# Performance work log

Measured on AMD Instinct MI355X. Metric: run time of the kernel, lower is better.

The kernel has to match this reference:

```python
import jax, jax.numpy as jnp
import numpy as np

N_NODES = 50000
N_EDGES = 1_600_000
IN_DIM = 6
EMB = 64
EDGE_DIM = 1
L = 4
BN_EPS = 1e-5


def _bn_relu(x, gamma, beta):
    # BatchNorm1d in training mode: biased batch stats over the row dim.
    mu = jnp.mean(x, axis=0)
    var = jnp.var(x, axis=0)
    xhat = (x - mu) * jax.lax.rsqrt(var + BN_EPS)
    return jax.nn.relu(xhat * gamma + beta)


def setup_inputs() -> dict:
    key = jax.random.key(0)
    ks = jax.random.split(key, 32)
    s = 0.1
    inp = {
        "x": jax.random.normal(ks[0], (N_NODES, IN_DIM), jnp.float32),
        "edge_index": jax.random.randint(ks[1], (2, N_EDGES), 0, N_NODES),
        "edge_attr": jax.random.normal(ks[2], (N_EDGES, EDGE_DIM), jnp.float32),
        "lin_in_W": jax.random.normal(ks[3], (IN_DIM, EMB)) * s,
        "lin_in_b": jnp.zeros((EMB,)),
        # per-layer stacked params, leading dim L
        "msg_W1": jax.random.normal(ks[4], (L, 2 * EMB + EDGE_DIM, EMB)) * s,
        "msg_b1": jnp.zeros((L, EMB)),
        "msg_g1": jnp.ones((L, EMB)),
        "msg_be1": jnp.zeros((L, EMB)),
        "msg_W2": jax.random.normal(ks[5], (L, EMB, EMB)) * s,
        "msg_b2": jnp.zeros((L, EMB)),
        "msg_g2": jnp.ones((L, EMB)),
        "msg_be2": jnp.zeros((L, EMB)),
        "upd_W1": jax.random.normal(ks[6], (L, 2 * EMB, EMB)) * s,
        "upd_b1": jnp.zeros((L, EMB)),
        "upd_g1": jnp.ones((L, EMB)),
        "upd_be1": jnp.zeros((L, EMB)),
        "upd_W2": jax.random.normal(ks[7], (L, EMB, EMB)) * s,
        "upd_b2": jnp.zeros((L, EMB)),
        "upd_g2": jnp.ones((L, EMB)),
        "upd_be2": jnp.zeros((L, EMB)),
        "pred_W": jax.random.normal(ks[8], (EMB, 1)) * s,
        "pred_b": jnp.zeros((1,)),
    }
    return inp


def reference(x, edge_index, edge_attr, lin_in_W, lin_in_b,
              msg_W1, msg_b1, msg_g1, msg_be1, msg_W2, msg_b2, msg_g2, msg_be2,
              upd_W1, upd_b1, upd_g1, upd_be1, upd_W2, upd_b2, upd_g2, upd_be2,
              pred_W, pred_b):
    n = x.shape[0]
    src = edge_index[0]  # j (source)
    dst = edge_index[1]  # i (target / aggregation index)

    h = x @ lin_in_W + lin_in_b  # (n, d)
    for l in range(L):
        h_i = h[dst]                              # (e, d) destination feats
        h_j = h[src]                              # (e, d) source feats
        m = jnp.concatenate([h_i, h_j, edge_attr], axis=-1)  # (e, 2d+de)
        m = _bn_relu(m @ msg_W1[l] + msg_b1[l], msg_g1[l], msg_be1[l])
        m = _bn_relu(m @ msg_W2[l] + msg_b2[l], msg_g2[l], msg_be2[l])
        aggr = jax.ops.segment_sum(m, dst, num_segments=n)   # (n, d)
        u = jnp.concatenate([h, aggr], axis=-1)              # (n, 2d)
        u = _bn_relu(u @ upd_W1[l] + upd_b1[l], upd_g1[l], upd_be1[l])
        u = _bn_relu(u @ upd_W2[l] + upd_b2[l], upd_g2[l], upd_be2[l])
        h = h + u  # residual
    out = h @ pred_W + pred_b
    return out.reshape(-1)
```

## Files before the change

### kernel.cpp

```cpp
#include <hip/hip_runtime.h>
#include <hip/hip_bf16.h>


#define BN_EPS 1e-5f
#define NSH 128
#define LYS 72
#define LW1S 168
#define LW2S 68
#define ASW 66

typedef __attribute__((ext_vector_type(8))) short short8;
typedef __attribute__((ext_vector_type(16))) float floatx16;

#define MFMA32 __builtin_amdgcn_mfma_f32_32x32x16_bf16

__device__ __forceinline__ short f2bs(float f) {
  union { float f; unsigned u; } x; x.f = f;
  unsigned r = x.u + 0x7fffu + ((x.u >> 16) & 1u);
  return (short)(r >> 16);
}
__device__ __forceinline__ short f2bs_fast(float f) {
  union { float f; unsigned u; } x; x.f = f;
  return (short)((x.u + 0x8000u) >> 16);
}
__device__ __forceinline__ float bs2f(short s) {
  union { unsigned u; float f; } x;
  x.u = ((unsigned)(unsigned short)s) << 16;
  return x.f;
}


__global__ void lin_in_kernel(const float* __restrict__ x,
                              const float* __restrict__ W,
                              const float* __restrict__ b, float* __restrict__ h,
                              short* __restrict__ hb, int N) {
  int gid = blockIdx.x * blockDim.x + threadIdx.x;
  if (gid >= N * 64) return;
  int n = gid >> 6, o = gid & 63;
  float acc = b[o];
#pragma unroll
  for (int k = 0; k < 6; ++k) acc += x[n * 6 + k] * W[k * 64 + o];
  h[gid] = acc;
  hb[gid] = f2bs(acc);
}

__global__ void deg_kernel(const int* __restrict__ ei, int* __restrict__ deg,
                           int E) {
  int gid = blockIdx.x * blockDim.x + threadIdx.x;
  if (gid < E) atomicAdd(&deg[ei[E + gid]], 1);
}

__global__ void scan_kernel(const int* __restrict__ deg, int* __restrict__ offs,
                            int N) {
  __shared__ int s[1024];
  int t = threadIdx.x;
  int chunk = (N + 1023) >> 10;
  int lo = t * chunk, hi = lo + chunk;
  if (hi > N) hi = N;
  if (lo > N) lo = N;
  int tot = 0;
  for (int i = lo; i < hi; ++i) tot += deg[i];
  s[t] = tot;
  __syncthreads();
  for (int off = 1; off < 1024; off <<= 1) {
    int v = (t >= off) ? s[t - off] : 0;
    __syncthreads();
    s[t] += v;
    __syncthreads();
  }
  int run = s[t] - tot;
  for (int i = lo; i < hi; ++i) {
    offs[i] = run;
    run += deg[i];
  }
}

__global__ void fill_kernel(const int* __restrict__ ei,
                            const int* __restrict__ offs, int* __restrict__ cnt,
                            int* __restrict__ sorted, int E) {
  int gid = blockIdx.x * blockDim.x + threadIdx.x;
  if (gid >= E) return;
  int d = ei[E + gid];
  int pos = offs[d] + atomicAdd(&cnt[d], 1);
  sorted[pos] = gid;
}

__global__ void gather_edges_kernel(const int* __restrict__ ei,
                                    const int* __restrict__ sorted,
                                    const float* __restrict__ ea,
                                    int* __restrict__ dd, int* __restrict__ ds,
                                    short* __restrict__ es, int E, int Epad) {
  int i = blockIdx.x * 256 + threadIdx.x;
  if (i >= Epad) return;
  if (i < E) {
    int e = sorted[i];
    dd[i] = ei[E + e];
    ds[i] = ei[e];
    es[i] = f2bs(ea[e]);
  } else {
    dd[i] = -1;
    ds[i] = 0;
    es[i] = 0;
  }
}

__global__ void pack_w1_kernel(const float* __restrict__ W,
                               short* __restrict__ Wt, int L_) {
  int i = blockIdx.x * 256 + threadIdx.x;
  if (i >= L_ * 64 * 160) return;
  int k = i % 160, n = (i / 160) % 64, l = i / (160 * 64);
  Wt[i] = (k < 129) ? f2bs(W[((size_t)l * 129 + k) * 64 + n]) : (short)0;
}

__global__ void pack_w2_kernel(const float* __restrict__ W,
                               short* __restrict__ Wt, int L_) {
  int i = blockIdx.x * 256 + threadIdx.x;
  if (i >= L_ * 64 * 64) return;
  int k = i % 64, n = (i / 64) % 64, l = i / 4096;
  Wt[i] = f2bs(W[((size_t)l * 64 + k) * 64 + n]);
}

__global__ void bn_finalize_kernel(const float* __restrict__ shards,
                                   const float* __restrict__ gamma,
                                   const float* __restrict__ beta, float cnt,
                                   float* __restrict__ ac) {
  int o = threadIdx.x;
  float s = 0.f, q = 0.f;
  for (int i = 0; i < NSH; ++i) {
    s += shards[i * 128 + o];
    q += shards[i * 128 + 64 + o];
  }
  float mu = s / cnt;
  float var = fmaxf(q / cnt - mu * mu, 0.f);
  float r = rsqrtf(var + BN_EPS);
  float g = gamma[o];
  ac[o] = g * r;
  ac[64 + o] = beta[o] - mu * g * r;
}

__global__ void bn_finalize_pack1(const float* __restrict__ shards,
                                  const float* __restrict__ gamma,
                                  const float* __restrict__ beta, float cnt,
                                  const float* __restrict__ W,
                                  const float* __restrict__ b,
                                  short* __restrict__ Wt,
                                  float* __restrict__ bs) {
  __shared__ float sa[64];
  int t = threadIdx.x;
  if (t < 64) {
    float s = 0.f, q = 0.f;
    for (int i = 0; i < NSH; ++i) {
      s += shards[i * 128 + t];
      q += shards[i * 128 + 64 + t];
    }
    float mu = s / cnt;
    float var = fmaxf(q / cnt - mu * mu, 0.f);
    float r = rsqrtf(var + BN_EPS);
    float a = gamma[t] * r;
    float c = beta[t] - mu * a;
    sa[t] = a;
    if (blockIdx.x == 0) bs[t] = a * b[t] + c;
  }
  __syncthreads();
  int i = blockIdx.x * 256 + t;
  if (i < 64 * 160) {
    int k = i % 160, n = i / 160;
    Wt[i] = (k < 129) ? f2bs(W[k * 64 + n] * sa[n]) : (short)0;
  }
}

__global__ void bn_finalize_pack2(const float* __restrict__ shards,
                                  const float* __restrict__ gamma,
                                  const float* __restrict__ beta, float cnt,
                                  const float* __restrict__ W,
                                  const float* __restrict__ b,
                                  short* __restrict__ Wt,
                                  float* __restrict__ bs) {
  __shared__ float sa[64];
  int t = threadIdx.x;
  if (t < 64) {
    float s = 0.f, q = 0.f;
    for (int i = 0; i < NSH; ++i) {
      s += shards[i * 128 + t];
      q += shards[i * 128 + 64 + t];
    }
    float mu = s / cnt;
    float var = fmaxf(q / cnt - mu * mu, 0.f);
    float r = rsqrtf(var + BN_EPS);
    float a = gamma[t] * r;
    float c = beta[t] - mu * a;
    sa[t] = a;
    if (blockIdx.x == 0) bs[t] = a * b[t] + c;
  }
  __syncthreads();
  int i = blockIdx.x * 256 + t;
  if (i < 64 * 64) {
    int k = i % 64, n = i / 64;
    Wt[i] = f2bs(W[k * 64 + n] * sa[n]);
  }
}


__device__ __forceinline__ void stage_w1(const short* __restrict__ Wt,
                                         short* Lw, int t) {
#pragma unroll
  for (int i = 0; i < 5; ++i) {
    int c = t + i * 256;
    int col = c / 20, ch = c % 20;
    *(short8*)&Lw[col * LW1S + ch * 8] = *(const short8*)&Wt[col * 160 + ch * 8];
  }
}
__device__ __forceinline__ void stage_w2(const short* __restrict__ Wt,
                                         short* Lw, int t) {
#pragma unroll
  for (int i = 0; i < 2; ++i) {
    int c = t + i * 256;
    int col = c >> 3, ch = c & 7;
    *(short8*)&Lw[col * LW2S + ch * 8] = *(const short8*)&Wt[col * 64 + ch * 8];
  }
}

__device__ __forceinline__ void gemm1_32(const short* __restrict__ hbf,
                                         const short* Lw1,
                                         const float* __restrict__ bias, int d,
                                         int sx, short eav, int me, int hl,
                                         floatx16 acc[2]) {
  const short* hd = hbf + (size_t)d * 64 + hl * 8;
  const short* hs = hbf + (size_t)sx * 64 + hl * 8;
  short8 A[8];
#pragma unroll
  for (int kc = 0; kc < 4; ++kc) A[kc] = *(const short8*)(hd + kc * 16);
#pragma unroll
  for (int kc = 0; kc < 4; ++kc) A[4 + kc] = *(const short8*)(hs + kc * 16);
  short8 a8 = {0, 0, 0, 0, 0, 0, 0, 0};
  if (hl == 0) a8[0] = eav;
#pragma unroll
  for (int nt = 0; nt < 2; ++nt) {
    int col = nt * 32 + me;
    float bv = bias[col];
    floatx16 a;
#pragma unroll
    for (int r = 0; r < 16; ++r) a[r] = bv;
    const short* wp = Lw1 + col * LW1S + hl * 8;
#pragma unroll
    for (int kc = 0; kc < 8; ++kc) {
      short8 B = *(const short8*)(wp + kc * 16);
      a = MFMA32(A[kc], B, a, 0, 0, 0);
    }
    short8 B8 = *(const short8*)(wp + 128);
    a = MFMA32(a8, B8, a, 0, 0, 0);
    acc[nt] = a;
  }
}

__device__ __forceinline__ void gemm2_32(const short* Ly, const short* Lw2,
                                         const float* __restrict__ bias, int w,
                                         int me, int hl, floatx16 acc[2]) {
  short8 Z[4];
  const short* zp = &Ly[(w * 32 + me) * LYS + hl * 8];
#pragma unroll
  for (int kc = 0; kc < 4; ++kc) Z[kc] = *(const short8*)(zp + kc * 16);
#pragma unroll
  for (int nt = 0; nt < 2; ++nt) {
    int col = nt * 32 + me;
    float bv = bias[col];
    floatx16 a;
#pragma unroll
    for (int r = 0; r < 16; ++r) a[r] = bv;
    const short* wp = Lw2 + col * LW2S + hl * 8;
#pragma unroll
    for (int kc = 0; kc < 4; ++kc) {
      short8 B = *(const short8*)(wp + kc * 16);
      a = MFMA32(Z[kc], B, a, 0, 0, 0);
    }
    acc[nt] = a;
  }
}

__device__ __forceinline__ void stats32(const floatx16 acc[2], int idx0, int w,
                                        int hl, int lane, int E, bool full,
                                        float* sredw) {
#pragma unroll
  for (int nt = 0; nt < 2; ++nt) {
    float s = 0.f, q = 0.f;
#pragma unroll
    for (int r = 0; r < 16; ++r) {
      float v = acc[nt][r];
      if (!full) {
        int row = (r & 3) + 8 * (r >> 2) + 4 * hl;
        if (idx0 + w * 32 + row >= E) v = 0.f;
      }
      s += v;
      q += v * v;
    }
    s += __shfl_down(s, 32, 64);
    q += __shfl_down(q, 32, 64);
    if (lane < 32) {
      sredw[nt * 32 + lane] = s;
      sredw[64 + nt * 32 + lane] = q;
    }
  }
}

__device__ __forceinline__ void write_ly(short* Ly, const floatx16 acc[2],
                                         int w, int me, int hl, bool mask,
                                         int idx0, int E) {
#pragma unroll
  for (int nt = 0; nt < 2; ++nt) {
    int col = nt * 32 + me;
#pragma unroll
    for (int r = 0; r < 16; ++r) {
      int row = (r & 3) + 8 * (r >> 2) + 4 * hl;
      float v = fmaxf(acc[nt][r], 0.f);
      if (mask && idx0 + w * 32 + row >= E) v = 0.f;
      Ly[(w * 32 + row) * LYS + col] = f2bs_fast(v);
    }
  }
}


__global__ __launch_bounds__(256) void edge_pass_a(
    const short* __restrict__ hbf, const short* __restrict__ Wt1,
    const float* __restrict__ b1, const int* __restrict__ dd,
    const int* __restrict__ dsr, const short* __restrict__ es,
    float* __restrict__ stat, int E) {
  __shared__ __align__(16) short Lw1[64 * LW1S];
  __shared__ float sred[4][128];
  int t = threadIdx.x, idx0 = blockIdx.x * 128;
  stage_w1(Wt1, Lw1, t);
  __syncthreads();
  int w = t >> 6, lane = t & 63, me = lane & 31, hl = lane >> 5;
  int eg = idx0 + w * 32 + me;
  int d = dd[eg];
  int dc = d < 0 ? 0 : d;
  int sx = dsr[eg];
  short eav = es[eg];
  floatx16 acc[2];
  gemm1_32(hbf, Lw1, b1, dc, sx, eav, me, hl, acc);
  bool full = idx0 + 128 <= E;
  stats32(acc, idx0, w, hl, lane, E, full, sred[w]);
  __syncthreads();
  if (t < 128) {
    float v = sred[0][t] + sred[1][t] + sred[2][t] + sred[3][t];
    atomicAdd(&stat[(size_t)(blockIdx.x & (NSH - 1)) * 128 + t], v);
  }
}

__global__ __launch_bounds__(256) void edge_pass_b(
    const short* __restrict__ hbf, const short* __restrict__ Wt1s,
    const float* __restrict__ b1s, const int* __restrict__ dd,
    const int* __restrict__ dsr, const short* __restrict__ es,
    const short* __restrict__ Wt2, const float* __restrict__ b2,
    float* __restrict__ stat, int E) {
  __shared__ __align__(16) short Lw1[64 * LW1S];
  __shared__ __align__(16) short Lw2[64 * LW2S];
  __shared__ __align__(16) short Ly[128 * LYS];
  __shared__ float sred[4][128];
  int t = threadIdx.x, idx0 = blockIdx.x * 128;
  stage_w1(Wt1s, Lw1, t);
  stage_w2(Wt2, Lw2, t);
  __syncthreads();
  int w = t >> 6, lane = t & 63, me = lane & 31, hl = lane >> 5;
  int eg = idx0 + w * 32 + me;
  int d = dd[eg];
  int dc = d < 0 ? 0 : d;
  int sx = dsr[eg];
  short eav = es[eg];
  floatx16 acc[2];
  gemm1_32(hbf, Lw1, b1s, dc, sx, eav, me, hl, acc);
  write_ly(Ly, acc, w, me, hl, false, idx0, E);
  floatx16 acc2[2];
  gemm2_32(Ly, Lw2, b2, w, me, hl, acc2);
  bool full = idx0 + 128 <= E;
  stats32(acc2, idx0, w, hl, lane, E, full, sred[w]);
  __syncthreads();
  if (t < 128) {
    float v = sred[0][t] + sred[1][t] + sred[2][t] + sred[3][t];
    atomicAdd(&stat[(size_t)(blockIdx.x & (NSH - 1)) * 128 + t], v);
  }
}

__global__ __launch_bounds__(256) void edge_pass_c(
    const short* __restrict__ hbf, const short* __restrict__ Wt1s,
    const float* __restrict__ b1s, const int* __restrict__ dd,
    const int* __restrict__ dsr, const short* __restrict__ es,
    const short* __restrict__ Wt2s, const float* __restrict__ b2s,
    float* __restrict__ aggr, int E) {
  __shared__ __align__(16) short Lw1[64 * LW1S];
  __shared__ __align__(16) short Lw2[64 * LW2S];
  __shared__ __align__(16) short Ly[128 * LYS];
  __shared__ int sdst[128];
  int t = threadIdx.x, idx0 = blockIdx.x * 128;
  if (t < 128) sdst[t] = dd[idx0 + t];
  stage_w1(Wt1s, Lw1, t);
  stage_w2(Wt2s, Lw2, t);
  __syncthreads();
  int w = t >> 6, lane = t & 63, me = lane & 31, hl = lane >> 5;
  int eg = idx0 + w * 32 + me;
  int d = sdst[w * 32 + me];
  int dc = d < 0 ? 0 : d;
  int sx = dsr[eg];
  short eav = es[eg];
  floatx16 acc[2];
  gemm1_32(hbf, Lw1, b1s, dc, sx, eav, me, hl, acc);
  write_ly(Ly, acc, w, me, hl, false, idx0, E);
  floatx16 acc2[2];
  gemm2_32(Ly, Lw2, b2s, w, me, hl, acc2);
  bool full = idx0 + 128 <= E;
  write_ly(Ly, acc2, w, me, hl, !full, idx0, E);
  __syncthreads();
  int scol = t & 63, g = t >> 6;
  float s = 0.f;
  int e0 = g * 32;
  for (int e = e0; e < e0 + 32; ++e) {
    int d2 = sdst[e];
    s += bs2f(Ly[e * LYS + scol]);
    int dn = (e == e0 + 31) ? -2 : sdst[e + 1];
    if (d2 != dn) {
      if (d2 >= 0) atomicAdd(&aggr[(size_t)d2 * 64 + scol], s);
      s = 0.f;
    }
  }
}


__device__ __forceinline__ void gemm_r2c8(const float* __restrict__ As,
                                          const float* __restrict__ W, int K,
                                          int rg, int cg, float acc[2][8]) {
  const float* ap = As + rg * 2;
  const float* wp = W + cg * 8;
#pragma unroll 4
  for (int k = 0; k < K; ++k) {
    float2 a = *(const float2*)&ap[k * ASW];
    float4 w0 = *(const float4*)&wp[k * 64];
    float4 w1 = *(const float4*)&wp[k * 64 + 4];
    float wv[8] = {w0.x, w0.y, w0.z, w0.w, w1.x, w1.y, w1.z, w1.w};
#pragma unroll
    for (int j = 0; j < 8; ++j) {
      acc[0][j] += a.x * wv[j];
      acc[1][j] += a.y * wv[j];
    }
  }
}

__device__ __forceinline__ void stats_r2c8(const float acc[2][8],
                                           float* __restrict__ shard, int t,
                                           int cg) {
  float s[8], q[8];
#pragma unroll
  for (int j = 0; j < 8; ++j) {
    s[j] = acc[0][j] + acc[1][j];
    q[j] = acc[0][j] * acc[0][j] + acc[1][j] * acc[1][j];
  }
#pragma unroll
  for (int off = 32; off >= 8; off >>= 1) {
#pragma unroll
    for (int j = 0; j < 8; ++j) {
      s[j] += __shfl_down(s[j], off, 64);
      q[j] += __shfl_down(q[j], off, 64);
    }
  }
  if (((t & 63) >> 3) == 0) {
#pragma unroll
    for (int j = 0; j < 8; ++j) {
      atomicAdd(&shard[cg * 8 + j], s[j]);
      atomicAdd(&shard[64 + cg * 8 + j], q[j]);
    }
  }
}

__global__ __launch_bounds__(256) void node_gemm1_v3(
    const float* __restrict__ h, const float* __restrict__ aggr,
    const float* __restrict__ W, const float* __restrict__ b,
    float* __restrict__ u1, float* __restrict__ stat, int N) {
  __shared__ __align__(16) float As[128 * ASW];
  int n0 = blockIdx.x * 64;
  int t = threadIdx.x;
  int c = t & 63, g = t >> 6;
  for (int n = g; n < 64; n += 4) {
    int idx = n0 + n;
    bool v = idx < N;
    As[c * ASW + n] = v ? h[(size_t)idx * 64 + c] : 0.f;
    As[(64 + c) * ASW + n] = v ? aggr[(size_t)idx * 64 + c] : 0.f;
  }
  __syncthreads();
  int rg = t >> 3, cg = t & 7;
  float acc[2][8];
#pragma unroll
  for (int i = 0; i < 2; ++i)
#pragma unroll
    for (int j = 0; j < 8; ++j) acc[i][j] = b[cg * 8 + j];
  gemm_r2c8(As, W, 128, rg, cg, acc);
#pragma unroll
  for (int i = 0; i < 2; ++i) {
    int idx = n0 + rg * 2 + i;
    if (idx < N) {
      *(float4*)&u1[(size_t)idx * 64 + cg * 8] =
          make_float4(acc[i][0], acc[i][1], acc[i][2], acc[i][3]);
      *(float4*)&u1[(size_t)idx * 64 + cg * 8 + 4] =
          make_float4(acc[i][4], acc[i][5], acc[i][6], acc[i][7]);
    } else {
#pragma unroll
      for (int j = 0; j < 8; ++j) acc[i][j] = 0.f;
    }
  }
  stats_r2c8(acc, stat + (size_t)(blockIdx.x & (NSH - 1)) * 128, t, cg);
}

__global__ __launch_bounds__(256) void node_gemm2_v3(
    const float* __restrict__ u1, const float* __restrict__ ac,
    const float* __restrict__ W, const float* __restrict__ b,
    float* __restrict__ u2, float* __restrict__ stat, int N) {
  __shared__ __align__(16) float As[64 * ASW];
  int n0 = blockIdx.x * 64;
  int t = threadIdx.x;
  int c = t & 63, g = t >> 6;
  float a1 = ac[c], c1 = ac[64 + c];
  for (int n = g; n < 64; n += 4) {
    int idx = n0 + n;
    bool v = idx < N;
    As[c * ASW + n] = v ? fmaxf(u1[(size_t)idx * 64 + c] * a1 + c1, 0.f) : 0.f;
  }
  __syncthreads();
  int rg = t >> 3, cg = t & 7;
  float acc[2][8];
#pragma unroll
  for (int i = 0; i < 2; ++i)
#pragma unroll
    for (int j = 0; j < 8; ++j) acc[i][j] = b[cg * 8 + j];
  gemm_r2c8(As, W, 64, rg, cg, acc);
#pragma unroll
  for (int i = 0; i < 2; ++i) {
    int idx = n0 + rg * 2 + i;
    if (idx < N) {
      *(float4*)&u2[(size_t)idx * 64 + cg * 8] =
          make_float4(acc[i][0], acc[i][1], acc[i][2], acc[i][3]);
      *(float4*)&u2[(size_t)idx * 64 + cg * 8 + 4] =
          make_float4(acc[i][4], acc[i][5], acc[i][6], acc[i][7]);
    } else {
#pragma unroll
      for (int j = 0; j < 8; ++j) acc[i][j] = 0.f;
    }
  }
  stats_r2c8(acc, stat + (size_t)(blockIdx.x & (NSH - 1)) * 128, t, cg);
}

__global__ void residual_kernel(float* __restrict__ h, short* __restrict__ hb,
                                const float* __restrict__ u2,
                                const float* __restrict__ ac, int total) {
  int gid = blockIdx.x * blockDim.x + threadIdx.x;
  if (gid >= total) return;
  int o = gid & 63;
  float v = u2[gid] * ac[o] + ac[64 + o];
  float nv = h[gid] + fmaxf(v, 0.f);
  h[gid] = nv;
  hb[gid] = f2bs(nv);
}

__global__ void pred_kernel(const float* __restrict__ h,
                            const float* __restrict__ W,
                            const float* __restrict__ b,
                            float* __restrict__ out, int N) {
  int n = blockIdx.x * blockDim.x + threadIdx.x;
  if (n >= N) return;
  float acc = b[0];
  const float* hr = h + (size_t)n * 64;
#pragma unroll
  for (int o = 0; o < 64; ++o) acc += hr[o] * W[o];
  out[n] = acc;
}


extern "C" void kernel_launch(void* const* d_in, const int* in_sizes, int n_in,
                              void* d_out, int out_size, void* d_ws,
                              size_t ws_size, hipStream_t stream) {
  const float* x = (const float*)d_in[0];
  const int* ei = (const int*)d_in[1];
  const float* ea = (const float*)d_in[2];
  const float* lin_W = (const float*)d_in[3];
  const float* lin_b = (const float*)d_in[4];
  const float* msg_W1 = (const float*)d_in[5];
  const float* msg_b1 = (const float*)d_in[6];
  const float* msg_g1 = (const float*)d_in[7];
  const float* msg_be1 = (const float*)d_in[8];
  const float* msg_W2 = (const float*)d_in[9];
  const float* msg_b2 = (const float*)d_in[10];
  const float* msg_g2 = (const float*)d_in[11];
  const float* msg_be2 = (const float*)d_in[12];
  const float* upd_W1 = (const float*)d_in[13];
  const float* upd_b1 = (const float*)d_in[14];
  const float* upd_g1 = (const float*)d_in[15];
  const float* upd_be1 = (const float*)d_in[16];
  const float* upd_W2 = (const float*)d_in[17];
  const float* upd_b2 = (const float*)d_in[18];
  const float* upd_g2 = (const float*)d_in[19];
  const float* upd_be2 = (const float*)d_in[20];
  const float* pred_W = (const float*)d_in[21];
  const float* pred_b = (const float*)d_in[22];
  float* out = (float*)d_out;

  const int N = in_sizes[0] / 6;
  const int E = in_sizes[1] / 2;
  const int L = 4;
  const int Epad = ((E + 127) / 128) * 128;

  char* p = (char*)d_ws;
  auto alloc = [&](size_t bytes) {
    void* r = (void*)p;
    p += (bytes + 255) & ~(size_t)255;
    return r;
  };
  float* h = (float*)alloc((size_t)N * 64 * 4);
  short* hb = (short*)alloc((size_t)N * 64 * 2);
  float* aggr = (float*)alloc((size_t)N * 64 * 4);
  float* u1 = (float*)alloc((size_t)N * 64 * 4);
  float* u2 = (float*)alloc((size_t)N * 64 * 4);
  float* stats = (float*)alloc((size_t)4 * NSH * 128 * 4);
  float* acu1 = (float*)alloc(128 * 4);
  float* acu2 = (float*)alloc(128 * 4);
  float* b1s = (float*)alloc(64 * 4);
  float* b2s = (float*)alloc(64 * 4);
  int* deg = (int*)alloc((size_t)N * 4);
  int* offs = (int*)alloc((size_t)N * 4);
  int* cnt = (int*)alloc((size_t)N * 4);
  int* sorted = (int*)alloc((size_t)E * 4);
  int* dd = (int*)alloc((size_t)Epad * 4);
  int* dsr = (int*)alloc((size_t)Epad * 4);
  short* es = (short*)alloc((size_t)Epad * 2);
  short* Wt1 = (short*)alloc((size_t)L * 64 * 160 * 2);
  short* Wt2 = (short*)alloc((size_t)L * 64 * 64 * 2);
  short* Wt1s = (short*)alloc((size_t)64 * 160 * 2);
  short* Wt2s = (short*)alloc((size_t)64 * 64 * 2);

  const int B = 256;
  const size_t REG = (size_t)NSH * 128;
  int gridE256 = (E + 255) / 256;
  int gridEb = Epad / 128;
  int gridM64 = (N + 63) / 64;
  int gridN64 = (N * 64 + B - 1) / B;
  int gridN = (N + B - 1) / B;

  hipMemsetAsync(deg, 0, (size_t)N * 4, stream);
  hipMemsetAsync(cnt, 0, (size_t)N * 4, stream);
  lin_in_kernel<<<gridN64, B, 0, stream>>>(x, lin_W, lin_b, h, hb, N);
  deg_kernel<<<gridE256, B, 0, stream>>>(ei, deg, E);
  scan_kernel<<<1, 1024, 0, stream>>>(deg, offs, N);
  fill_kernel<<<gridE256, B, 0, stream>>>(ei, offs, cnt, sorted, E);
  gather_edges_kernel<<<(Epad + 255) / 256, B, 0, stream>>>(ei, sorted, ea, dd,
                                                            dsr, es, E, Epad);
  pack_w1_kernel<<<(L * 64 * 160 + 255) / 256, B, 0, stream>>>(msg_W1, Wt1, L);
  pack_w2_kernel<<<(L * 64 * 64 + 255) / 256, B, 0, stream>>>(msg_W2, Wt2, L);

  for (int l = 0; l < L; ++l) {
    const short* Wt1l = Wt1 + (size_t)l * 64 * 160;
    const short* Wt2l = Wt2 + (size_t)l * 64 * 64;
    const float* U1 = upd_W1 + (size_t)l * 128 * 64;
    const float* U2 = upd_W2 + (size_t)l * 64 * 64;
    hipMemsetAsync(stats, 0, (size_t)4 * REG * 4, stream);
    hipMemsetAsync(aggr, 0, (size_t)N * 64 * 4, stream);
    edge_pass_a<<<gridEb, 256, 0, stream>>>(hb, Wt1l, msg_b1 + l * 64, dd, dsr,
                                            es, stats, E);
    bn_finalize_pack1<<<(64 * 160 + 255) / 256, B, 0, stream>>>(
        stats, msg_g1 + l * 64, msg_be1 + l * 64, (float)E,
        msg_W1 + (size_t)l * 129 * 64, msg_b1 + l * 64, Wt1s, b1s);
    edge_pass_b<<<gridEb, 256, 0, stream>>>(hb, Wt1s, b1s, dd, dsr, es, Wt2l,
                                            msg_b2 + l * 64, stats + REG, E);
    bn_finalize_pack2<<<(64 * 64 + 255) / 256, B, 0, stream>>>(
        stats + REG, msg_g2 + l * 64, msg_be2 + l * 64, (float)E,
        msg_W2 + (size_t)l * 64 * 64, msg_b2 + l * 64, Wt2s, b2s);
    edge_pass_c<<<gridEb, 256, 0, stream>>>(hb, Wt1s, b1s, dd, dsr, es, Wt2s,
                                            b2s, aggr, E);
    node_gemm1_v3<<<gridM64, 256, 0, stream>>>(h, aggr, U1, upd_b1 + l * 64,
                                               u1, stats + 2 * REG, N);
    bn_finalize_kernel<<<1, 64, 0, stream>>>(stats + 2 * REG, upd_g1 + l * 64,
                                             upd_be1 + l * 64, (float)N, acu1);
    node_gemm2_v3<<<gridM64, 256, 0, stream>>>(u1, acu1, U2, upd_b2 + l * 64,
                                               u2, stats + 3 * REG, N);
    bn_finalize_kernel<<<1, 64, 0, stream>>>(stats + 3 * REG, upd_g2 + l * 64,
                                             upd_be2 + l * 64, (float)N, acu2);
    residual_kernel<<<gridN64, B, 0, stream>>>(h, hb, u2, acu2, N * 64);
  }
  pred_kernel<<<gridN, B, 0, stream>>>(h, pred_W, pred_b, out, N);
}
```

Baseline: 2.082 ms.

## Process multiple edge tiles per block and transpose first GEMM for register-side aggregation

Result: faster. 1.937 ms (-7.0%).

```diff
diff --git a/kernel.cpp b/kernel.cpp
--- a/kernel.cpp
+++ b/kernel.cpp
@@ -4,11 +4,13 @@
 
 #define BN_EPS 1e-5f
 #define NSH 128
+#define TPB 4
 #define LYS 72
 #define LW1S 168
 #define LW2S 68
 #define ASW 66
 
+typedef __attribute__((ext_vector_type(4))) short short4v;
 typedef __attribute__((ext_vector_type(8))) short short8;
 typedef __attribute__((ext_vector_type(16))) float floatx16;
 
@@ -253,11 +255,59 @@
   }
 }
 
-__device__ __forceinline__ void gemm2_32(const short* Ly, const short* Lw2,
+__device__ __forceinline__ void gemm1T_32(const short* __restrict__ hbf,
+                                          const short* Lw1, int d, int sx,
+                                          short eav, int me, int hl,
+                                          floatx16 acc[2]) {
+  const short* hd = hbf + (size_t)d * 64 + hl * 8;
+  const short* hs = hbf + (size_t)sx * 64 + hl * 8;
+  short8 Bf[8];
+#pragma unroll
+  for (int kc = 0; kc < 4; ++kc) Bf[kc] = *(const short8*)(hd + kc * 16);
+#pragma unroll
+  for (int kc = 0; kc < 4; ++kc) Bf[4 + kc] = *(const short8*)(hs + kc * 16);
+  short8 b8 = {0, 0, 0, 0, 0, 0, 0, 0};
+  if (hl == 0) b8[0] = eav;
+#pragma unroll
+  for (int nt = 0; nt < 2; ++nt) {
+    floatx16 a;
+#pragma unroll
+    for (int r = 0; r < 16; ++r) a[r] = 0.f;
+    const short* wp = Lw1 + (nt * 32 + me) * LW1S + hl * 8;
+#pragma unroll
+    for (int kc = 0; kc < 8; ++kc) {
+      short8 A = *(const short8*)(wp + kc * 16);
+      a = MFMA32(A, Bf[kc], a, 0, 0, 0);
+    }
+    short8 A8 = *(const short8*)(wp + 128);
+    a = MFMA32(A8, b8, a, 0, 0, 0);
+    acc[nt] = a;
+  }
+}
+
+__device__ __forceinline__ void write_z(short* Lz, const floatx16 acc[2],
+                                        const float b1v[2][16], int w, int me,
+                                        int hl) {
+#pragma unroll
+  for (int nt = 0; nt < 2; ++nt)
+#pragma unroll
+    for (int g4 = 0; g4 < 4; ++g4) {
+      int n1b = nt * 32 + 8 * g4 + 4 * hl;
+      short4v pk;
+#pragma unroll
+      for (int j = 0; j < 4; ++j) {
+        int r = g4 * 4 + j;
+        pk[j] = f2bs_fast(fmaxf(acc[nt][r] + b1v[nt][r], 0.f));
+      }
+      *(short4v*)&Lz[(w * 32 + me) * LYS + n1b] = pk;
+    }
+}
+
+__device__ __forceinline__ void gemm2_32(const short* Lz, const short* Lw2,
                                          const float* __restrict__ bias, int w,
                                          int me, int hl, floatx16 acc[2]) {
   short8 Z[4];
-  const short* zp = &Ly[(w * 32 + me) * LYS + hl * 8];
+  const short* zp = &Lz[(w * 32 + me) * LYS + hl * 8];
 #pragma unroll
   for (int kc = 0; kc < 4; ++kc) Z[kc] = *(const short8*)(zp + kc * 16);
 #pragma unroll
@@ -277,9 +327,9 @@
   }
 }
 
-__device__ __forceinline__ void stats32(const floatx16 acc[2], int idx0, int w,
-                                        int hl, int lane, int E, bool full,
-                                        float* sredw) {
+__device__ __forceinline__ void stats32_acc(const floatx16 acc[2], int idx0,
+                                            int w, int hl, int E, bool full,
+                                            float sa[2], float qa[2]) {
 #pragma unroll
   for (int nt = 0; nt < 2; ++nt) {
     float s = 0.f, q = 0.f;
@@ -295,26 +345,28 @@
     }
     s += __shfl_down(s, 32, 64);
     q += __shfl_down(q, 32, 64);
-    if (lane < 32) {
-      sredw[nt * 32 + lane] = s;
-      sredw[64 + nt * 32 + lane] = q;
-    }
-  }
-}
-
-__device__ __forceinline__ void write_ly(short* Ly, const floatx16 acc[2],
-                                         int w, int me, int hl, bool mask,
-                                         int idx0, int E) {
-#pragma unroll
-  for (int nt = 0; nt < 2; ++nt) {
-    int col = nt * 32 + me;
-#pragma unroll
-    for (int r = 0; r < 16; ++r) {
-      int row = (r & 3) + 8 * (r >> 2) + 4 * hl;
-      float v = fmaxf(acc[nt][r], 0.f);
-      if (mask && idx0 + w * 32 + row >= E) v = 0.f;
-      Ly[(w * 32 + row) * LYS + col] = f2bs_fast(v);
-    }
+    sa[nt] += s;
+    qa[nt] += q;
+  }
+}
+
+__device__ __forceinline__ void stats_epilogue(float sred[4][128],
+                                               const float sa[2],
+                                               const float qa[2], int w,
+                                               int lane, int t,
+                                               float* __restrict__ stat,
+                                               int shard) {
+  if (lane < 32) {
+#pragma unroll
+    for (int nt = 0; nt < 2; ++nt) {
+      sred[w][nt * 32 + lane] = sa[nt];
+      sred[w][64 + nt * 32 + lane] = qa[nt];
+    }
+  }
+  __syncthreads();
+  if (t < 128) {
+    float v = sred[0][t] + sred[1][t] + sred[2][t] + sred[3][t];
+    atomicAdd(&stat[(size_t)shard * 128 + t], v);
   }
 }
 
@@ -323,27 +375,27 @@
     const short* __restrict__ hbf, const short* __restrict__ Wt1,
     const float* __restrict__ b1, const int* __restrict__ dd,
     const int* __restrict__ dsr, const short* __restrict__ es,
-    float* __restrict__ stat, int E) {
+    float* __restrict__ stat, int E, int Epad) {
   __shared__ __align__(16) short Lw1[64 * LW1S];
   __shared__ float sred[4][128];
-  int t = threadIdx.x, idx0 = blockIdx.x * 128;
+  int t = threadIdx.x;
   stage_w1(Wt1, Lw1, t);
   __syncthreads();
   int w = t >> 6, lane = t & 63, me = lane & 31, hl = lane >> 5;
-  int eg = idx0 + w * 32 + me;
-  int d = dd[eg];
-  int dc = d < 0 ? 0 : d;
-  int sx = dsr[eg];
-  short eav = es[eg];
-  floatx16 acc[2];
-  gemm1_32(hbf, Lw1, b1, dc, sx, eav, me, hl, acc);
-  bool full = idx0 + 128 <= E;
-  stats32(acc, idx0, w, hl, lane, E, full, sred[w]);
-  __syncthreads();
-  if (t < 128) {
-    float v = sred[0][t] + sred[1][t] + sred[2][t] + sred[3][t];
-    atomicAdd(&stat[(size_t)(blockIdx.x & (NSH - 1)) * 128 + t], v);
-  }
+  float sa[2] = {0.f, 0.f}, qa[2] = {0.f, 0.f};
+  for (int it = 0; it < TPB; ++it) {
+    int idx0 = (blockIdx.x * TPB + it) * 128;
+    if (idx0 >= Epad) break;
+    int eg = idx0 + w * 32 + me;
+    int d = dd[eg];
+    int dc = d < 0 ? 0 : d;
+    int sx = dsr[eg];
+    short eav = es[eg];
+    floatx16 acc[2];
+    gemm1_32(hbf, Lw1, b1, dc, sx, eav, me, hl, acc);
+    stats32_acc(acc, idx0, w, hl, E, idx0 + 128 <= E, sa, qa);
+  }
+  stats_epilogue(sred, sa, qa, w, lane, t, stat, blockIdx.x & (NSH - 1));
 }
 
 __global__ __launch_bounds__(256) void edge_pass_b(
@@ -351,33 +403,39 @@
     const float* __restrict__ b1s, const int* __restrict__ dd,
     const int* __restrict__ dsr, const short* __restrict__ es,
     const short* __restrict__ Wt2, const float* __restrict__ b2,
-    float* __restrict__ stat, int E) {
+    float* __restrict__ stat, int E, int Epad) {
   __shared__ __align__(16) short Lw1[64 * LW1S];
   __shared__ __align__(16) short Lw2[64 * LW2S];
-  __shared__ __align__(16) short Ly[128 * LYS];
+  __shared__ __align__(16) short Lz[128 * LYS];
   __shared__ float sred[4][128];
-  int t = threadIdx.x, idx0 = blockIdx.x * 128;
+  int t = threadIdx.x;
   stage_w1(Wt1s, Lw1, t);
   stage_w2(Wt2, Lw2, t);
   __syncthreads();
   int w = t >> 6, lane = t & 63, me = lane & 31, hl = lane >> 5;
-  int eg = idx0 + w * 32 + me;
-  int d = dd[eg];
-  int dc = d < 0 ? 0 : d;
-  int sx = dsr[eg];
-  short eav = es[eg];
-  floatx16 acc[2];
-  gemm1_32(hbf, Lw1, b1s, dc, sx, eav, me, hl, acc);
-  write_ly(Ly, acc, w, me, hl, false, idx0, E);
-  floatx16 acc2[2];
-  gemm2_32(Ly, Lw2, b2, w, me, hl, acc2);
-  bool full = idx0 + 128 <= E;
-  stats32(acc2, idx0, w, hl, lane, E, full, sred[w]);
-  __syncthreads();
-  if (t < 128) {
-    float v = sred[0][t] + sred[1][t] + sred[2][t] + sred[3][t];
-    atomicAdd(&stat[(size_t)(blockIdx.x & (NSH - 1)) * 128 + t], v);
-  }
+  float b1v[2][16];
+#pragma unroll
+  for (int nt = 0; nt < 2; ++nt)
+#pragma unroll
+    for (int r = 0; r < 16; ++r)
+      b1v[nt][r] = b1s[nt * 32 + (r & 3) + 8 * (r >> 2) + 4 * hl];
+  float sa[2] = {0.f, 0.f}, qa[2] = {0.f, 0.f};
+  for (int it = 0; it < TPB; ++it) {
+    int idx0 = (blockIdx.x * TPB + it) * 128;
+    if (idx0 >= Epad) break;
+    int eg = idx0 + w * 32 + me;
+    int d = dd[eg];
+    int dc = d < 0 ? 0 : d;
+    int sx = dsr[eg];
+    short eav = es[eg];
+    floatx16 acc[2];
+    gemm1T_32(hbf, Lw1, dc, sx, eav, me, hl, acc);
+    write_z(Lz, acc, b1v, w, me, hl);
+    floatx16 acc2[2];
+    gemm2_32(Lz, Lw2, b2, w, me, hl, acc2);
+    stats32_acc(acc2, idx0, w, hl, E, idx0 + 128 <= E, sa, qa);
+  }
+  stats_epilogue(sred, sa, qa, w, lane, t, stat, blockIdx.x & (NSH - 1));
 }
 
 __global__ __launch_bounds__(256) void edge_pass_c(
@@ -385,41 +443,65 @@
     const float* __restrict__ b1s, const int* __restrict__ dd,
     const int* __restrict__ dsr, const short* __restrict__ es,
     const short* __restrict__ Wt2s, const float* __restrict__ b2s,
-    float* __restrict__ aggr, int E) {
+    float* __restrict__ aggr, int E, int Epad) {
   __shared__ __align__(16) short Lw1[64 * LW1S];
   __shared__ __align__(16) short Lw2[64 * LW2S];
-  __shared__ __align__(16) short Ly[128 * LYS];
+  __shared__ __align__(16) short Lz[128 * LYS];
   __shared__ int sdst[128];
-  int t = threadIdx.x, idx0 = blockIdx.x * 128;
-  if (t < 128) sdst[t] = dd[idx0 + t];
+  int t = threadIdx.x;
   stage_w1(Wt1s, Lw1, t);
   stage_w2(Wt2s, Lw2, t);
   __syncthreads();
   int w = t >> 6, lane = t & 63, me = lane & 31, hl = lane >> 5;
-  int eg = idx0 + w * 32 + me;
-  int d = sdst[w * 32 + me];
-  int dc = d < 0 ? 0 : d;
-  int sx = dsr[eg];
-  short eav = es[eg];
-  floatx16 acc[2];
-  gemm1_32(hbf, Lw1, b1s, dc, sx, eav, me, hl, acc);
-  write_ly(Ly, acc, w, me, hl, false, idx0, E);
-  floatx16 acc2[2];
-  gemm2_32(Ly, Lw2, b2s, w, me, hl, acc2);
-  bool full = idx0 + 128 <= E;
-  write_ly(Ly, acc2, w, me, hl, !full, idx0, E);
-  __syncthreads();
-  int scol = t & 63, g = t >> 6;
-  float s = 0.f;
-  int e0 = g * 32;
-  for (int e = e0; e < e0 + 32; ++e) {
-    int d2 = sdst[e];
-    s += bs2f(Ly[e * LYS + scol]);
-    int dn = (e == e0 + 31) ? -2 : sdst[e + 1];
-    if (d2 != dn) {
-      if (d2 >= 0) atomicAdd(&aggr[(size_t)d2 * 64 + scol], s);
-      s = 0.f;
-    }
+  float b1v[2][16];
+#pragma unroll
+  for (int nt = 0; nt < 2; ++nt)
+#pragma unroll
+    for (int r = 0; r < 16; ++r)
+      b1v[nt][r] = b1s[nt * 32 + (r & 3) + 8 * (r >> 2) + 4 * hl];
+  for (int it = 0; it < TPB; ++it) {
+    int idx0 = (blockIdx.x * TPB + it) * 128;
+    if (idx0 >= Epad) break;
+    if (t < 128) sdst[t] = dd[idx0 + t];
+    int eg = idx0 + w * 32 + me;
+    int d = dd[eg];
+    int dc = d < 0 ? 0 : d;
+    int sx = dsr[eg];
+    short eav = es[eg];
+    floatx16 acc[2];
+    gemm1T_32(hbf, Lw1, dc, sx, eav, me, hl, acc);
+    write_z(Lz, acc, b1v, w, me, hl);
+    floatx16 acc2[2];
+    gemm2_32(Lz, Lw2, b2s, w, me, hl, acc2);
+    __syncthreads();
+    int sb = w * 32;
+    float s0 = 0.f, s1 = 0.f;
+    int d2 = sdst[sb + 4 * hl];
+#pragma unroll
+    for (int g4 = 0; g4 < 4; ++g4) {
+#pragma unroll
+      for (int j = 0; j < 4; ++j) {
+        int r = g4 * 4 + j;
+        s0 += fmaxf(acc2[0][r], 0.f);
+        s1 += fmaxf(acc2[1][r], 0.f);
+        int offn;
+        if (j == 3)
+          offn = (g4 == 3) ? -1 : 8 * (g4 + 1) + 4 * hl;
+        else
+          offn = 8 * g4 + 4 * hl + j + 1;
+        int dn = (offn < 0) ? -2 : sdst[sb + offn];
+        if (d2 != dn) {
+          if (d2 >= 0) {
+            atomicAdd(&aggr[(size_t)d2 * 64 + me], s0);
+            atomicAdd(&aggr[(size_t)d2 * 64 + me + 32], s1);
+          }
+          s0 = 0.f;
+          s1 = 0.f;
+        }
+        d2 = dn;
+      }
+    }
+    __syncthreads();
   }
 }
 
@@ -613,13 +695,13 @@
   float* h = (float*)alloc((size_t)N * 64 * 4);
   short* hb = (short*)alloc((size_t)N * 64 * 2);
   float* aggr = (float*)alloc((size_t)N * 64 * 4);
-  float* u1 = (float*)alloc((size_t)N * 64 * 4);
-  float* u2 = (float*)alloc((size_t)N * 64 * 4);
   float* stats = (float*)alloc((size_t)4 * NSH * 128 * 4);
   float* acu1 = (float*)alloc(128 * 4);
   float* acu2 = (float*)alloc(128 * 4);
   float* b1s = (float*)alloc(64 * 4);
   float* b2s = (float*)alloc(64 * 4);
+  float* u1 = (float*)alloc((size_t)N * 64 * 4);
+  float* u2 = (float*)alloc((size_t)N * 64 * 4);
   int* deg = (int*)alloc((size_t)N * 4);
   int* offs = (int*)alloc((size_t)N * 4);
   int* cnt = (int*)alloc((size_t)N * 4);
@@ -635,7 +717,8 @@
   const int B = 256;
   const size_t REG = (size_t)NSH * 128;
   int gridE256 = (E + 255) / 256;
-  int gridEb = Epad / 128;
+  int NT = Epad / 128;
+  int gridEdge = (NT + TPB - 1) / TPB;
   int gridM64 = (N + 63) / 64;
   int gridN64 = (N * 64 + B - 1) / B;
   int gridN = (N + B - 1) / B;
@@ -656,20 +739,20 @@
     const short* Wt2l = Wt2 + (size_t)l * 64 * 64;
     const float* U1 = upd_W1 + (size_t)l * 128 * 64;
     const float* U2 = upd_W2 + (size_t)l * 64 * 64;
-    hipMemsetAsync(stats, 0, (size_t)4 * REG * 4, stream);
-    hipMemsetAsync(aggr, 0, (size_t)N * 64 * 4, stream);
-    edge_pass_a<<<gridEb, 256, 0, stream>>>(hb, Wt1l, msg_b1 + l * 64, dd, dsr,
-                                            es, stats, E);
+    hipMemsetAsync(aggr, 0, (size_t)N * 64 * 4 + (size_t)4 * REG * 4, stream);
+    edge_pass_a<<<gridEdge, 256, 0, stream>>>(hb, Wt1l, msg_b1 + l * 64, dd,
+                                              dsr, es, stats, E, Epad);
     bn_finalize_pack1<<<(64 * 160 + 255) / 256, B, 0, stream>>>(
         stats, msg_g1 + l * 64, msg_be1 + l * 64, (float)E,
         msg_W1 + (size_t)l * 129 * 64, msg_b1 + l * 64, Wt1s, b1s);
-    edge_pass_b<<<gridEb, 256, 0, stream>>>(hb, Wt1s, b1s, dd, dsr, es, Wt2l,
-                                            msg_b2 + l * 64, stats + REG, E);
+    edge_pass_b<<<gridEdge, 256, 0, stream>>>(hb, Wt1s, b1s, dd, dsr, es, Wt2l,
+                                              msg_b2 + l * 64, stats + REG, E,
+                                              Epad);
     bn_finalize_pack2<<<(64 * 64 + 255) / 256, B, 0, stream>>>(
         stats + REG, msg_g2 + l * 64, msg_be2 + l * 64, (float)E,
         msg_W2 + (size_t)l * 64 * 64, msg_b2 + l * 64, Wt2s, b2s);
-    edge_pass_c<<<gridEb, 256, 0, stream>>>(hb, Wt1s, b1s, dd, dsr, es, Wt2s,
-                                            b2s, aggr, E);
+    edge_pass_c<<<gridEdge, 256, 0, stream>>>(hb, Wt1s, b1s, dd, dsr, es, Wt2s,
+                                              b2s, aggr, E, Epad);
     node_gemm1_v3<<<gridM64, 256, 0, stream>>>(h, aggr, U1, upd_b1 + l * 64,
                                                u1, stats + 2 * REG, N);
     bn_finalize_kernel<<<1, 64, 0, stream>>>(stats + 2 * REG, upd_g1 + l * 64,
```
